# Kernel optimization log

Hardware: AMD Instinct MI355X
Metric: run time of the kernel (lower is better)

Reference implementation:

```python
import jax, jax.numpy as jnp
import numpy as np

N, K, M = 4096, 4096, 12288  # tokens, in_features, out_features


def setup_inputs() -> dict:
    key = jax.random.key(0)
    k1, k2, k3, k4, k5 = jax.random.split(key, 5)
    x = jax.random.randint(k1, (N, K), -127, 128, dtype=jnp.int32)
    weight = jax.random.randint(k2, (M, K), -127, 128, dtype=jnp.int32)
    # per-token input scale and per-output-channel dequant scale (small positive)
    input_scale = jax.random.uniform(k3, (N,), dtype=jnp.float32) * 0.01 + 1e-4
    dequant_scale = jax.random.uniform(k4, (M,), dtype=jnp.float32) * 0.01 + 1e-4
    bias = jax.random.normal(k5, (M,), dtype=jnp.float32)
    return {"x": x, "weight": weight, "input_scale": input_scale,
            "dequant_scale": dequant_scale, "bias": bias}


def reference(x, weight, input_scale, dequant_scale, bias):
    # int8 GEMM with int32 accumulation: acc[n, m] = sum_k x[n,k] * w[m,k]
    acc = jnp.matmul(x, weight.T)  # [N, M] int32
    # fused dequant: per-token scale * per-channel scale, then bias add
    out = acc.astype(jnp.float32) * input_scale[:, None] * dequant_scale[None, :] + bias[None, :]
    return out
```

## Files before the change

kernel.cpp:

```cpp
#include <hip/hip_runtime.h>
#include <cstdint>
#include <cstddef>

#define N_TOK 4096
#define K_DIM 4096
#define M_DIM 12288

using i32x4 = __attribute__((ext_vector_type(4))) int;

constexpr long CHUNKS_X = ((long)N_TOK * K_DIM) / 16;
constexpr long CHUNKS_W = ((long)M_DIM * K_DIM) / 16;
constexpr long CHUNKS_TOTAL = CHUNKS_X + CHUNKS_W;

__global__ __launch_bounds__(256) void pack_i8_kernel(
    const int* __restrict__ x, const int* __restrict__ w,
    int8_t* __restrict__ x8, int8_t* __restrict__ w8)
{
  long idx = (long)blockIdx.x * 256 + threadIdx.x;
  const int* src;
  int8_t* dst;
  if (idx < CHUNKS_X) { src = x + idx * 16; dst = x8 + idx * 16; }
  else { long j = idx - CHUNKS_X; src = w + j * 16; dst = w8 + j * 16; }
  i32x4 v0 = *(const i32x4*)(src);
  i32x4 v1 = *(const i32x4*)(src + 4);
  i32x4 v2 = *(const i32x4*)(src + 8);
  i32x4 v3 = *(const i32x4*)(src + 12);
  auto pack4 = [](i32x4 v) -> int {
    return (int)((unsigned)(v.x & 0xff)        | ((unsigned)(v.y & 0xff) << 8) |
                 ((unsigned)(v.z & 0xff) << 16) | ((unsigned)(v.w & 0xff) << 24));
  };
  i32x4 o;
  o.x = pack4(v0); o.y = pack4(v1); o.z = pack4(v2); o.w = pack4(v3);
  *(i32x4*)dst = o;
}

#define BM 128
#define BN 128
#define BK 128
#define GRID_M (N_TOK / BM)
#define GRID_N (M_DIM / BN)
#define NWG (GRID_M * GRID_N)
#define KT (K_DIM / BK)

__device__ __forceinline__ void load_lds16(const void* g, void* l) {
  __builtin_amdgcn_global_load_lds(
      (const __attribute__((address_space(1))) void*)g,
      (__attribute__((address_space(3))) void*)l, 16, 0, 0);
}

__global__ __launch_bounds__(256, 2) void w8a8_gemm_kernel(
    const int8_t* __restrict__ A8,
    const int8_t* __restrict__ B8,
    const float* __restrict__ input_scale,
    const float* __restrict__ dequant_scale,
    const float* __restrict__ bias,
    float* __restrict__ out)
{
  __shared__ int8_t As[2][BM * BK];
  __shared__ int8_t Bs[2][BN * BK];

  const int tid  = threadIdx.x;
  const int lane = tid & 63;
  const int wid  = tid >> 6;
  const int wr   = wid >> 1;
  const int wc   = wid & 1;
  const int lr   = lane & 15;
  const int lg   = lane >> 4;
  const int xr   = (lr & 7) << 4;

  int bid = blockIdx.x;
  int w_  = (bid & 7) * (NWG / 8) + (bid >> 3);
  const int GROUP = 8;
  const int width = GROUP * GRID_N;
  int gid = w_ / width;
  int rem = w_ % width;
  int bm  = gid * GROUP + (rem % GROUP);
  int bn  = rem / GROUP;
  const int brow = bm * BM;
  const int bcol = bn * BN;

  auto stage = [&](int buf, int kt) {
    const int k0 = kt * BK;
#pragma unroll
    for (int t = 0; t < 4; ++t) {
      int c = t * 256 + tid;
      int row = c >> 3;
      int slot = (c & 7) ^ (row & 7);
      load_lds16(A8 + (size_t)(brow + row) * K_DIM + k0 + slot * 16,
                 &As[buf][c * 16]);
    }
#pragma unroll
    for (int t = 0; t < 4; ++t) {
      int c = t * 256 + tid;
      int row = c >> 3;
      int slot = (c & 7) ^ (row & 7);
      load_lds16(B8 + (size_t)(bcol + row) * K_DIM + k0 + slot * 16,
                 &Bs[buf][c * 16]);
    }
  };

  i32x4 acc[4][4] = {};

  stage(0, 0);
  for (int kt = 0; kt < KT; ++kt) {
    const int cur = kt & 1;
    __syncthreads();
    if (kt + 1 < KT) stage(cur ^ 1, kt + 1);
#pragma unroll
    for (int s = 0; s < 2; ++s) {
      i32x4 a[4], b[4];
#pragma unroll
      for (int i = 0; i < 4; ++i)
        a[i] = *(const i32x4*)&As[cur][(wr * 64 + i * 16 + lr) * BK +
                                       ((s * 64 + lg * 16) ^ xr)];
#pragma unroll
      for (int j = 0; j < 4; ++j)
        b[j] = *(const i32x4*)&Bs[cur][(wc * 64 + j * 16 + lr) * BK +
                                       ((s * 64 + lg * 16) ^ xr)];
#pragma unroll
      for (int i = 0; i < 4; ++i)
#pragma unroll
        for (int j = 0; j < 4; ++j)
          acc[i][j] = __builtin_amdgcn_mfma_i32_16x16x64_i8(a[i], b[j],
                                                            acc[i][j], 0, 0, 0);
    }
  }

  const int orow = brow + wr * 64;
  const int ocol = bcol + wc * 64 + lr;
  float isc[4][4];
#pragma unroll
  for (int i = 0; i < 4; ++i)
#pragma unroll
    for (int r = 0; r < 4; ++r)
      isc[i][r] = input_scale[orow + i * 16 + lg * 4 + r];

#pragma unroll
  for (int j = 0; j < 4; ++j) {
    const int m = ocol + j * 16;
    const float dsc = dequant_scale[m];
    const float bs  = bias[m];
#pragma unroll
    for (int i = 0; i < 4; ++i) {
#pragma unroll
      for (int r = 0; r < 4; ++r) {
        const int n = orow + i * 16 + lg * 4 + r;
        out[(size_t)n * M_DIM + m] = (float)acc[i][j][r] * isc[i][r] * dsc + bs;
      }
    }
  }
}

extern "C" void kernel_launch(void* const* d_in, const int* in_sizes, int n_in,
                              void* d_out, int out_size, void* d_ws, size_t ws_size,
                              hipStream_t stream) {
  const int*   x             = (const int*)d_in[0];
  const int*   w             = (const int*)d_in[1];
  const float* input_scale   = (const float*)d_in[2];
  const float* dequant_scale = (const float*)d_in[3];
  const float* bias          = (const float*)d_in[4];
  float*       out           = (float*)d_out;

  int8_t* x8 = (int8_t*)d_ws;
  int8_t* w8 = x8 + (size_t)N_TOK * K_DIM;

  pack_i8_kernel<<<(int)(CHUNKS_TOTAL / 256), 256, 0, stream>>>(x, w, x8, w8);
  w8a8_gemm_kernel<<<NWG, 256, 0, stream>>>(x8, w8, input_scale, dequant_scale,
                                            bias, out);
}
```

Baseline: 610.2 us.

## Use 256x256 tiles with a 512-thread, sub-tile-interleaved LDS prefetch pipeline

The GEMM moves from 128x128 tiles with 256 threads to 256x256 tiles with 512 threads and a single 128KB LDS buffer. Each K tile is split into 64-wide halves, and global-to-LDS loads for upcoming halves are interleaved between MFMA groups using explicit barriers, s_setprio and hand-placed vmcnt waits. The aim is to raise operand reuse per byte loaded and hide global-load latency behind matrix math. The pack kernel also becomes a grid-stride loop writing one packed int per group of four. In exchange, occupancy drops to one block per CU, and the hand-tuned waitcnt counts are fragile.

```diff
diff --git a/kernel.cpp b/kernel.cpp
--- a/kernel.cpp
+++ b/kernel.cpp
@@ -8,39 +8,26 @@
 
 using i32x4 = __attribute__((ext_vector_type(4))) int;
 
-constexpr long CHUNKS_X = ((long)N_TOK * K_DIM) / 16;
-constexpr long CHUNKS_W = ((long)M_DIM * K_DIM) / 16;
-constexpr long CHUNKS_TOTAL = CHUNKS_X + CHUNKS_W;
+constexpr long GROUPS_X     = (long)N_TOK * K_DIM / 4;
+constexpr long GROUPS_TOTAL = ((long)N_TOK + M_DIM) * K_DIM / 4;
 
 __global__ __launch_bounds__(256) void pack_i8_kernel(
-    const int* __restrict__ x, const int* __restrict__ w,
-    int8_t* __restrict__ x8, int8_t* __restrict__ w8)
-{
-  long idx = (long)blockIdx.x * 256 + threadIdx.x;
-  const int* src;
-  int8_t* dst;
-  if (idx < CHUNKS_X) { src = x + idx * 16; dst = x8 + idx * 16; }
-  else { long j = idx - CHUNKS_X; src = w + j * 16; dst = w8 + j * 16; }
-  i32x4 v0 = *(const i32x4*)(src);
-  i32x4 v1 = *(const i32x4*)(src + 4);
-  i32x4 v2 = *(const i32x4*)(src + 8);
-  i32x4 v3 = *(const i32x4*)(src + 12);
-  auto pack4 = [](i32x4 v) -> int {
-    return (int)((unsigned)(v.x & 0xff)        | ((unsigned)(v.y & 0xff) << 8) |
-                 ((unsigned)(v.z & 0xff) << 16) | ((unsigned)(v.w & 0xff) << 24));
-  };
-  i32x4 o;
-  o.x = pack4(v0); o.y = pack4(v1); o.z = pack4(v2); o.w = pack4(v3);
-  *(i32x4*)dst = o;
-}
-
-#define BM 128
-#define BN 128
-#define BK 128
+    const int* __restrict__ x, const int* __restrict__ w, int* __restrict__ out8)
+{
+  const long stride = (long)gridDim.x * 256;
+  for (long g = (long)blockIdx.x * 256 + threadIdx.x; g < GROUPS_TOTAL; g += stride) {
+    const int* src = (g < GROUPS_X) ? (x + g * 4) : (w + (g - GROUPS_X) * 4);
+    i32x4 v = *(const i32x4*)src;
+    out8[g] = (v.x & 0xff) | ((v.y & 0xff) << 8) | ((v.z & 0xff) << 16) | (v.w << 24);
+  }
+}
+
+#define BM 256
+#define BN 256
+#define KT 32
 #define GRID_M (N_TOK / BM)
 #define GRID_N (M_DIM / BN)
 #define NWG (GRID_M * GRID_N)
-#define KT (K_DIM / BK)
 
 __device__ __forceinline__ void load_lds16(const void* g, void* l) {
   __builtin_amdgcn_global_load_lds(
@@ -48,7 +35,119 @@
       (__attribute__((address_space(3))) void*)l, 16, 0, 0);
 }
 
-__global__ __launch_bounds__(256, 2) void w8a8_gemm_kernel(
+
+__device__ __forceinline__ void stage_region(
+    int8_t* lds, int buf, int ab, int s, int ktarg,
+    const int8_t* A8, const int8_t* B8, int brow, int bcol, int tid)
+{
+  const int8_t* gbase = ab ? (B8 + (size_t)bcol * K_DIM)
+                           : (A8 + (size_t)brow * K_DIM);
+  const int lb = (buf * 4 + ab * 2 + s) * 16384;
+  const int gk = ktarg * 128 + s * 64;
+#pragma unroll
+  for (int p = 0; p < 2; ++p) {
+    int c = p * 512 + tid;
+    int row  = c >> 2;
+    int slot = (c & 3) ^ (row & 3);
+    load_lds16(gbase + (size_t)row * K_DIM + gk + slot * 16,
+               lds + lb + c * 16);
+  }
+}
+
+template <int MODE>
+__device__ __forceinline__ void ktile(
+    int kt, int8_t* lds, const int8_t* A8, const int8_t* B8,
+    int brow, int bcol, int tid, int wr, int wc, int lr, int xs16,
+    i32x4 (&acc)[8][4])
+{
+  const int cur = kt & 1;
+  const int bA0 = (cur * 4 + 0) * 16384;
+  const int bA1 = (cur * 4 + 1) * 16384;
+  const int bB0 = (cur * 4 + 2) * 16384;
+  const int bB1 = (cur * 4 + 3) * 16384;
+  const int arow = wr * 128 + lr;
+  const int bcol_ = wc * 64 + lr;
+
+  i32x4 b[4];
+
+  {
+#pragma unroll
+    for (int j = 0; j < 4; ++j)
+      b[j] = *(const i32x4*)&lds[bB0 + (bcol_ + j * 16) * 64 + xs16];
+    i32x4 a[4];
+#pragma unroll
+    for (int i = 0; i < 4; ++i)
+      a[i] = *(const i32x4*)&lds[bA0 + (arow + i * 16) * 64 + xs16];
+    if (MODE >= 1) stage_region(lds, cur ^ 1, 0, 1, kt + 1, A8, B8, brow, bcol, tid);
+    __builtin_amdgcn_s_barrier();
+    __builtin_amdgcn_s_setprio(1);
+#pragma unroll
+    for (int i = 0; i < 4; ++i)
+#pragma unroll
+      for (int j = 0; j < 4; ++j)
+        acc[i][j] = __builtin_amdgcn_mfma_i32_16x16x64_i8(a[i], b[j], acc[i][j], 0, 0, 0);
+    __builtin_amdgcn_s_setprio(0);
+    __builtin_amdgcn_s_barrier();
+  }
+
+  {
+    i32x4 a[4];
+#pragma unroll
+    for (int i = 0; i < 4; ++i)
+      a[i] = *(const i32x4*)&lds[bA0 + (arow + (4 + i) * 16) * 64 + xs16];
+    if (MODE >= 1) stage_region(lds, cur ^ 1, 1, 1, kt + 1, A8, B8, brow, bcol, tid);
+    __builtin_amdgcn_s_barrier();
+    __builtin_amdgcn_s_setprio(1);
+#pragma unroll
+    for (int i = 0; i < 4; ++i)
+#pragma unroll
+      for (int j = 0; j < 4; ++j)
+        acc[4 + i][j] = __builtin_amdgcn_mfma_i32_16x16x64_i8(a[i], b[j], acc[4 + i][j], 0, 0, 0);
+    __builtin_amdgcn_s_setprio(0);
+    __builtin_amdgcn_s_barrier();
+  }
+
+  {
+#pragma unroll
+    for (int j = 0; j < 4; ++j)
+      b[j] = *(const i32x4*)&lds[bB1 + (bcol_ + j * 16) * 64 + xs16];
+    i32x4 a[4];
+#pragma unroll
+    for (int i = 0; i < 4; ++i)
+      a[i] = *(const i32x4*)&lds[bA1 + (arow + i * 16) * 64 + xs16];
+    if (MODE == 2) stage_region(lds, cur, 0, 0, kt + 2, A8, B8, brow, bcol, tid);
+    __builtin_amdgcn_s_barrier();
+    __builtin_amdgcn_s_setprio(1);
+#pragma unroll
+    for (int i = 0; i < 4; ++i)
+#pragma unroll
+      for (int j = 0; j < 4; ++j)
+        acc[i][j] = __builtin_amdgcn_mfma_i32_16x16x64_i8(a[i], b[j], acc[i][j], 0, 0, 0);
+    __builtin_amdgcn_s_setprio(0);
+    __builtin_amdgcn_s_barrier();
+  }
+
+  {
+    i32x4 a[4];
+#pragma unroll
+    for (int i = 0; i < 4; ++i)
+      a[i] = *(const i32x4*)&lds[bA1 + (arow + (4 + i) * 16) * 64 + xs16];
+    if (MODE == 2) stage_region(lds, cur, 1, 0, kt + 2, A8, B8, brow, bcol, tid);
+    __builtin_amdgcn_s_barrier();
+    __builtin_amdgcn_s_setprio(1);
+#pragma unroll
+    for (int i = 0; i < 4; ++i)
+#pragma unroll
+      for (int j = 0; j < 4; ++j)
+        acc[4 + i][j] = __builtin_amdgcn_mfma_i32_16x16x64_i8(a[i], b[j], acc[4 + i][j], 0, 0, 0);
+    __builtin_amdgcn_s_setprio(0);
+    if (MODE == 2)      asm volatile("s_waitcnt vmcnt(4)" ::: "memory");
+    else if (MODE == 1) asm volatile("s_waitcnt vmcnt(0)" ::: "memory");
+    __builtin_amdgcn_s_barrier();
+  }
+}
+
+__global__ __launch_bounds__(512, 2) void w8a8_gemm_kernel(
     const int8_t* __restrict__ A8,
     const int8_t* __restrict__ B8,
     const float* __restrict__ input_scale,
@@ -56,96 +155,55 @@
     const float* __restrict__ bias,
     float* __restrict__ out)
 {
-  __shared__ int8_t As[2][BM * BK];
-  __shared__ int8_t Bs[2][BN * BK];
+  __shared__ int8_t lds[131072];
 
   const int tid  = threadIdx.x;
   const int lane = tid & 63;
   const int wid  = tid >> 6;
-  const int wr   = wid >> 1;
-  const int wc   = wid & 1;
+  const int wr   = wid >> 2;
+  const int wc   = wid & 3;
   const int lr   = lane & 15;
   const int lg   = lane >> 4;
-  const int xr   = (lr & 7) << 4;
+  const int xs16 = ((lg ^ (lr & 3)) << 4);
 
   int bid = blockIdx.x;
   int w_  = (bid & 7) * (NWG / 8) + (bid >> 3);
-  const int GROUP = 8;
-  const int width = GROUP * GRID_N;
-  int gid = w_ / width;
-  int rem = w_ % width;
-  int bm  = gid * GROUP + (rem % GROUP);
-  int bn  = rem / GROUP;
+  const int width = 4 * GRID_N;
+  int gid = w_ / width, rem = w_ % width;
+  int bm = gid * 4 + (rem & 3);
+  int bn = rem >> 2;
   const int brow = bm * BM;
   const int bcol = bn * BN;
 
-  auto stage = [&](int buf, int kt) {
-    const int k0 = kt * BK;
-#pragma unroll
-    for (int t = 0; t < 4; ++t) {
-      int c = t * 256 + tid;
-      int row = c >> 3;
-      int slot = (c & 7) ^ (row & 7);
-      load_lds16(A8 + (size_t)(brow + row) * K_DIM + k0 + slot * 16,
-                 &As[buf][c * 16]);
-    }
-#pragma unroll
-    for (int t = 0; t < 4; ++t) {
-      int c = t * 256 + tid;
-      int row = c >> 3;
-      int slot = (c & 7) ^ (row & 7);
-      load_lds16(B8 + (size_t)(bcol + row) * K_DIM + k0 + slot * 16,
-                 &Bs[buf][c * 16]);
-    }
-  };
-
-  i32x4 acc[4][4] = {};
-
-  stage(0, 0);
-  for (int kt = 0; kt < KT; ++kt) {
-    const int cur = kt & 1;
-    __syncthreads();
-    if (kt + 1 < KT) stage(cur ^ 1, kt + 1);
-#pragma unroll
-    for (int s = 0; s < 2; ++s) {
-      i32x4 a[4], b[4];
-#pragma unroll
-      for (int i = 0; i < 4; ++i)
-        a[i] = *(const i32x4*)&As[cur][(wr * 64 + i * 16 + lr) * BK +
-                                       ((s * 64 + lg * 16) ^ xr)];
-#pragma unroll
-      for (int j = 0; j < 4; ++j)
-        b[j] = *(const i32x4*)&Bs[cur][(wc * 64 + j * 16 + lr) * BK +
-                                       ((s * 64 + lg * 16) ^ xr)];
-#pragma unroll
-      for (int i = 0; i < 4; ++i)
-#pragma unroll
-        for (int j = 0; j < 4; ++j)
-          acc[i][j] = __builtin_amdgcn_mfma_i32_16x16x64_i8(a[i], b[j],
-                                                            acc[i][j], 0, 0, 0);
-    }
-  }
-
-  const int orow = brow + wr * 64;
+  i32x4 acc[8][4] = {};
+
+  stage_region(lds, 0, 0, 0, 0, A8, B8, brow, bcol, tid);
+  stage_region(lds, 0, 1, 0, 0, A8, B8, brow, bcol, tid);
+  stage_region(lds, 0, 0, 1, 0, A8, B8, brow, bcol, tid);
+  stage_region(lds, 0, 1, 1, 0, A8, B8, brow, bcol, tid);
+  stage_region(lds, 1, 0, 0, 1, A8, B8, brow, bcol, tid);
+  stage_region(lds, 1, 1, 0, 1, A8, B8, brow, bcol, tid);
+  asm volatile("s_waitcnt vmcnt(4)" ::: "memory");
+  __builtin_amdgcn_s_barrier();
+
+  for (int kt = 0; kt < KT - 2; ++kt)
+    ktile<2>(kt, lds, A8, B8, brow, bcol, tid, wr, wc, lr, xs16, acc);
+  ktile<1>(KT - 2, lds, A8, B8, brow, bcol, tid, wr, wc, lr, xs16, acc);
+  ktile<0>(KT - 1, lds, A8, B8, brow, bcol, tid, wr, wc, lr, xs16, acc);
+
+  const int orow = brow + wr * 128;
   const int ocol = bcol + wc * 64 + lr;
-  float isc[4][4];
-#pragma unroll
-  for (int i = 0; i < 4; ++i)
-#pragma unroll
-    for (int r = 0; r < 4; ++r)
-      isc[i][r] = input_scale[orow + i * 16 + lg * 4 + r];
-
 #pragma unroll
   for (int j = 0; j < 4; ++j) {
     const int m = ocol + j * 16;
     const float dsc = dequant_scale[m];
     const float bs  = bias[m];
 #pragma unroll
-    for (int i = 0; i < 4; ++i) {
+    for (int fi = 0; fi < 8; ++fi) {
 #pragma unroll
       for (int r = 0; r < 4; ++r) {
-        const int n = orow + i * 16 + lg * 4 + r;
-        out[(size_t)n * M_DIM + m] = (float)acc[i][j][r] * isc[i][r] * dsc + bs;
+        const int n = orow + fi * 16 + lg * 4 + r;
+        out[(size_t)n * M_DIM + m] = (float)acc[fi][j][r] * input_scale[n] * dsc + bs;
       }
     }
   }
@@ -164,7 +222,7 @@
   int8_t* x8 = (int8_t*)d_ws;
   int8_t* w8 = x8 + (size_t)N_TOK * K_DIM;
 
-  pack_i8_kernel<<<(int)(CHUNKS_TOTAL / 256), 256, 0, stream>>>(x, w, x8, w8);
-  w8a8_gemm_kernel<<<NWG, 256, 0, stream>>>(x8, w8, input_scale, dequant_scale,
+  pack_i8_kernel<<<4096, 256, 0, stream>>>(x, w, (int*)d_ws);
+  w8a8_gemm_kernel<<<NWG, 512, 0, stream>>>(x8, w8, input_scale, dequant_scale,
                                             bias, out);
 }
```

Measured after the change: 567.9 us. -6.9%, faster.
